# Kernel optimization log

Measured on AMD Instinct MI355X. Metric: run time of the kernel, lower is better.

Reference implementation:

```python
import jax, jax.numpy as jnp
import numpy as np

D_MODEL = 1024
N_HEADS = 16
N_KV_HEADS = 4
D_K = D_MODEL // N_HEADS
Q_SIZE = D_MODEL
KV_SIZE = N_KV_HEADS * D_K
QKV_SIZE = Q_SIZE + 2 * KV_SIZE
EPS = 1.1920929e-07  # torch.nn.RMSNorm default eps (fp32 machine eps)
ROPE_BASE = 10000.0


def rms_norm(x, w):
    # normalize over last dim, learned scale (torch nn.RMSNorm)
    return x * jax.lax.rsqrt(jnp.mean(x * x, axis=-1, keepdims=True) + EPS) * w


def rope(x):
    # torchtune RotaryPositionalEmbeddings: interleaved pairs, x is [B,T,H,D]
    T, d = x.shape[1], x.shape[-1]
    inv_freq = 1.0 / (ROPE_BASE ** (jnp.arange(0, d, 2, dtype=jnp.float32) / d))
    ang = jnp.arange(T, dtype=jnp.float32)[:, None] * inv_freq[None, :]  # [T, d/2]
    cos = jnp.cos(ang)[None, :, None, :]
    sin = jnp.sin(ang)[None, :, None, :]
    xr = x.reshape(x.shape[:-1] + (d // 2, 2))
    x1, x2 = xr[..., 0], xr[..., 1]
    out = jnp.stack([x1 * cos - x2 * sin, x1 * sin + x2 * cos], axis=-1)
    return out.reshape(x.shape)


def setup_inputs() -> dict:
    key = jax.random.key(0)
    k1, k2 = jax.random.split(key)
    x = jax.random.normal(k1, (2, 2048, D_MODEL), dtype=jnp.float32)
    qkvo = jax.random.normal(k2, (QKV_SIZE + D_MODEL, D_MODEL), dtype=jnp.float32) * 0.02
    q_norm_w = jnp.ones((D_K,), dtype=jnp.float32)
    k_norm_w = jnp.ones((D_K,), dtype=jnp.float32)
    return {"x": x, "qkvo": qkvo, "q_norm_w": q_norm_w, "k_norm_w": k_norm_w}


def reference(x, qkvo, q_norm_w, k_norm_w):
    B, T, _ = x.shape
    groups = N_HEADS // N_KV_HEADS
    qkv = x @ qkvo[:QKV_SIZE].T  # [B,T,qkv_size]
    Q = qkv[..., :Q_SIZE].reshape(B, T, N_HEADS, D_K)
    K = qkv[..., Q_SIZE:Q_SIZE + KV_SIZE].reshape(B, T, N_KV_HEADS, D_K)
    V = qkv[..., Q_SIZE + KV_SIZE:].reshape(B, T, N_KV_HEADS, D_K)
    Q = rope(rms_norm(Q, q_norm_w))
    K = rope(rms_norm(K, k_norm_w))
    K = jnp.repeat(K, groups, axis=2)  # GQA expand to [B,T,H,D]
    V = jnp.repeat(V, groups, axis=2)
    scale = 1.0 / np.sqrt(D_K).astype(np.float32)
    scores = jnp.einsum('bqhd,bkhd->bhqk', Q, K) * scale
    causal = jnp.tril(jnp.ones((T, T), dtype=bool))
    scores = jnp.where(causal[None, None], scores, jnp.float32(-jnp.inf))
    attn = jax.nn.softmax(scores, axis=-1)
    out = jnp.einsum('bhqk,bkhd->bqhd', attn, V).reshape(B, T, D_MODEL)
    return out @ qkvo[QKV_SIZE:].T
```

## Files before the change

### kernel.cpp

```cpp
#include <hip/hip_runtime.h>
#include <hip/hip_bf16.h>
#include <cstdint>
#include <cstddef>

typedef __bf16 bf16x8 __attribute__((ext_vector_type(8)));
typedef float f32x4 __attribute__((ext_vector_type(4)));

__device__ __forceinline__ unsigned short f2bf(float f) {
    unsigned u = __builtin_bit_cast(unsigned, f);
    u += 0x7FFFu + ((u >> 16) & 1u);
    return (unsigned short)(u >> 16);
}
__device__ __forceinline__ unsigned pk2(float a, float b) {
    typedef __bf16 bf16x2 __attribute__((ext_vector_type(2)));
    bf16x2 h;
    h[0] = (__bf16)a;
    h[1] = (__bf16)b;
    unsigned r;
    __builtin_memcpy(&r, &h, 4);
    return r;
}
__device__ __forceinline__ float fexp2(float x) {
#if __has_builtin(__builtin_amdgcn_exp2f)
    return __builtin_amdgcn_exp2f(x);
#else
    return __expf(x * 0.6931471805599453f);
#endif
}
__device__ __forceinline__ void gld16(const void* g, void* l) {
    __builtin_amdgcn_global_load_lds((const __attribute__((address_space(1))) void*)g,
                                     (__attribute__((address_space(3))) void*)l, 16, 0, 0);
}

__global__ __launch_bounds__(256) void cast_kernel(const float4* __restrict__ x,
                                                   const float4* __restrict__ w,
                                                   ushort4* __restrict__ xbf,
                                                   ushort4* __restrict__ wbf) {
    int i = blockIdx.x * 256 + threadIdx.x;
    const int NX4 = 4096 * 1024 / 4;
    const int NW4 = 2560 * 1024 / 4;
    float4 v;
    ushort4* o;
    if (i < NX4) { v = x[i]; o = xbf + i; }
    else {
        int j = i - NX4;
        if (j >= NW4) return;
        v = w[j]; o = wbf + j;
    }
    ushort4 r;
    r.x = f2bf(v.x); r.y = f2bf(v.y); r.z = f2bf(v.z); r.w = f2bf(v.w);
    *o = r;
}

__global__ __launch_bounds__(256) void gemm_bf16(const ushort* __restrict__ A,
                                                 const ushort* __restrict__ B,
                                                 float* __restrict__ C,
                                                 int M, int N, int K) {
    __shared__ __align__(16) ushort LA[2][4096];
    __shared__ __align__(16) ushort LB[2][8192];
    int tid = threadIdx.x;
    int w = tid >> 6, lane = tid & 63;
    int qm = lane & 15, quad = lane >> 4;
    int m0 = blockIdx.x * 64, n0 = blockIdx.y * 128;
    int mw = (w & 1) * 32, nw = (w >> 1) * 64;
    int sw = qm & 7;

    f32x4 acc[2][4];
#pragma unroll
    for (int i = 0; i < 2; i++)
#pragma unroll
        for (int j = 0; j < 4; j++) acc[i][j] = (f32x4){0.f, 0.f, 0.f, 0.f};

    int sa[2], ra[2], ga[2];
#pragma unroll
    for (int u = 0; u < 2; u++) {
        sa[u] = tid + u * 256;
        ra[u] = sa[u] >> 3;
        ga[u] = (sa[u] & 7) ^ (ra[u] & 7);
    }
    int sb[4], rb[4], gb[4];
#pragma unroll
    for (int u = 0; u < 4; u++) {
        sb[u] = tid + u * 256;
        rb[u] = sb[u] >> 3;
        gb[u] = (sb[u] & 7) ^ (rb[u] & 7);
    }

    auto do_stage = [&](int k0, int buf) {
#pragma unroll
        for (int u = 0; u < 2; u++)
            gld16(A + (size_t)(m0 + ra[u]) * K + k0 + ga[u] * 8, &LA[buf][sa[u] * 8]);
#pragma unroll
        for (int u = 0; u < 4; u++)
            gld16(B + (size_t)(n0 + rb[u]) * K + k0 + gb[u] * 8, &LB[buf][sb[u] * 8]);
    };

    do_stage(0, 0);
    int buf = 0;
    for (int k0 = 0; k0 < K; k0 += 64, buf ^= 1) {
        __syncthreads();
        if (k0 + 64 < K) do_stage(k0 + 64, buf ^ 1);
        bf16x8 a[2][2], bb[4][2];
#pragma unroll
        for (int mi = 0; mi < 2; mi++)
#pragma unroll
            for (int h = 0; h < 2; h++)
                a[mi][h] = *(const bf16x8*)&LA[buf][((mw + mi * 16 + qm) * 8 + ((h * 4 + quad) ^ sw)) * 8];
#pragma unroll
        for (int ni = 0; ni < 4; ni++)
#pragma unroll
            for (int h = 0; h < 2; h++)
                bb[ni][h] = *(const bf16x8*)&LB[buf][((nw + ni * 16 + qm) * 8 + ((h * 4 + quad) ^ sw)) * 8];
#pragma unroll
        for (int h = 0; h < 2; h++)
#pragma unroll
            for (int mi = 0; mi < 2; mi++)
#pragma unroll
                for (int ni = 0; ni < 4; ni++)
                    acc[mi][ni] = __builtin_amdgcn_mfma_f32_16x16x32_bf16(a[mi][h], bb[ni][h], acc[mi][ni], 0, 0, 0);
    }
#pragma unroll
    for (int mi = 0; mi < 2; mi++)
#pragma unroll
        for (int ni = 0; ni < 4; ni++) {
            int row = m0 + mw + mi * 16 + quad * 4;
            int col = n0 + nw + ni * 16 + qm;
            float* cp = C + (size_t)row * N + col;
#pragma unroll
            for (int r = 0; r < 4; r++) cp[(size_t)r * N] = acc[mi][ni][r];
        }
}

__global__ __launch_bounds__(256) void normrope_kernel(const float* __restrict__ qkv,
                                                       const float* __restrict__ qw,
                                                       const float* __restrict__ kw,
                                                       ushort* __restrict__ Q,
                                                       ushort* __restrict__ Kb) {
    int r = blockIdx.x;
    int b = r >> 11;
    int t = r & 2047;
    int tid = threadIdx.x;
    int w = tid >> 6;
    int lane = tid & 63;

    float inv_freq = __expf(-((float)(lane & 62) * (1.0f / 64.0f)) * 9.210340371976184f);
    float sn, cs;
    sincosf((float)t * inv_freq, &sn, &cs);

#pragma unroll
    for (int hg = 0; hg < 5; hg++) {
        int col = hg * 256 + w * 64 + lane;
        float v = qkv[(size_t)r * 1536 + col];
        float ss = v * v;
#pragma unroll
        for (int m = 1; m < 64; m <<= 1) ss += __shfl_xor(ss, m);
        float rinv = rsqrtf(ss * (1.0f / 64.0f) + 1.1920929e-7f);
        float wt = (hg < 4) ? qw[lane] : kw[lane];
        float vn = v * rinv * wt;
        float pr = __shfl_xor(vn, 1);
        float out = (lane & 1) ? fmaf(pr, sn, vn * cs) : fmaf(vn, cs, -pr * sn);
        if (hg < 4) {
            int h = hg * 4 + w;
            Q[((size_t)(b * 16 + h) * 2048 + t) * 64 + lane] = f2bf(out * 0.125f);
        } else {
            Kb[((size_t)(b * 4 + w) * 2048 + t) * 64 + lane] = f2bf(out);
        }
    }
}

__global__ __launch_bounds__(256) void vtrans_kernel(const float* __restrict__ qkv,
                                                     ushort* __restrict__ VT) {
    __shared__ float tile[64][65];
    int bkv = blockIdx.x;
    int t0 = blockIdx.y * 64;
    int b = bkv >> 2;
    int kvh = bkv & 3;
    int tid = threadIdx.x;
    int c = tid & 63;
    int rr = tid >> 6;
#pragma unroll
    for (int p = 0; p < 16; p++) {
        int tl = p * 4 + rr;
        tile[tl][c] = qkv[((size_t)(b * 2048) + t0 + tl) * 1536 + 1280 + kvh * 64 + c];
    }
    __syncthreads();
    int w5 = c & 31;
    int pc = (c & 32) + ((w5 >> 2) & 3) * 8 + (w5 >> 4) * 4 + (w5 & 3);
#pragma unroll
    for (int p = 0; p < 16; p++) {
        int dd = p * 4 + rr;
        VT[((size_t)bkv * 64 + dd) * 2048 + t0 + pc] = f2bf(tile[c][dd]);
    }
}

__global__ __launch_bounds__(256) void attn7_kernel(const ushort* __restrict__ Q,
                                                    const ushort* __restrict__ K,
                                                    const ushort* __restrict__ VT,
                                                    ushort* __restrict__ O) {
    __shared__ __align__(16) ushort KT[2][4096];
    __shared__ __align__(16) ushort VL[2][4096];

    const float LOG2E = 1.4426950408889634f;
    const float C8 = 11.541560327111707f;

    int blk = blockIdx.x;
    int qp = 31 - (blk >> 5);
    int bh = blk & 31;
    int tid = threadIdx.x;
    int w = tid >> 6, lane = tid & 63;
    int qm = lane & 15, quad = lane >> 4;
    int b = bh >> 4, h = bh & 15;
    int bkv = b * 4 + (h >> 2);

    const ushort* Qbh = Q + (size_t)bh * 2048 * 64;
    const ushort* Kbh = K + (size_t)bkv * 2048 * 64;
    const ushort* Vbh = VT + (size_t)bkv * 64 * 2048;
    int sw = qm & 7;

    int s0 = tid, s1 = tid + 256;
    int r0 = s0 >> 3, g0 = (s0 & 7) ^ (r0 & 7);
    int r1 = s1 >> 3, g1 = (s1 & 7) ^ (r1 & 7);

    auto do_stage = [&](int j0, int buf) {
        gld16(Kbh + (size_t)(j0 + r0) * 64 + g0 * 8, &KT[buf][s0 * 8]);
        gld16(Kbh + (size_t)(j0 + r1) * 64 + g1 * 8, &KT[buf][s1 * 8]);
        gld16(Vbh + (size_t)r0 * 2048 + j0 + g0 * 8, &VL[buf][s0 * 8]);
        gld16(Vbh + (size_t)r1 * 2048 + j0 + g1 * 8, &VL[buf][s1 * 8]);
    };

    int nch = qp + 1;
    int q0 = qp * 64 + w * 16;
    const ushort* qptr = Qbh + (size_t)(q0 + qm) * 64 + quad * 8;
    bf16x8 qb0 = *(const bf16x8*)qptr;
    bf16x8 qb1 = *(const bf16x8*)(qptr + 32);
    f32x4 oacc[4];
    float lacc = 0.f;
#pragma unroll
    for (int i = 0; i < 4; i++) oacc[i] = (f32x4){0.f, 0.f, 0.f, 0.f};

    do_stage(0, 0);
    int buf = 0;
#pragma unroll 1
    for (int i = 0; i < nch; i++, buf ^= 1) {
        int j0 = i * 64;
        __syncthreads();
        if (i + 1 < nch) do_stage(j0 + 64, buf ^ 1);

        f32x4 st[4];
#pragma unroll
        for (int tj = 0; tj < 4; tj++) st[tj] = (f32x4){0.f, 0.f, 0.f, 0.f};
#pragma unroll
        for (int tj = 0; tj < 4; tj++) {
            bf16x8 kf0 = *(const bf16x8*)&KT[buf][((16 * tj + qm) * 8 + (quad ^ sw)) * 8];
            bf16x8 kf1 = *(const bf16x8*)&KT[buf][((16 * tj + qm) * 8 + ((4 + quad) ^ sw)) * 8];
            st[tj] = __builtin_amdgcn_mfma_f32_16x16x32_bf16(kf0, qb0, st[tj], 0, 0, 0);
            st[tj] = __builtin_amdgcn_mfma_f32_16x16x32_bf16(kf1, qb1, st[tj], 0, 0, 0);
        }
        if (i == nch - 1) {
#pragma unroll
            for (int tj = 0; tj < 4; tj++)
#pragma unroll
                for (int r = 0; r < 4; r++) {
                    int key = j0 + tj * 16 + quad * 4 + r;
                    if (key > q0 + qm) st[tj][r] = -1e30f;
                }
        }
        float rs = 0.f;
#pragma unroll
        for (int tj = 0; tj < 4; tj++)
#pragma unroll
            for (int r = 0; r < 4; r++) {
                float pv = fexp2(fmaf(st[tj][r], LOG2E, -C8));
                st[tj][r] = pv;
                rs += pv;
            }
        lacc += rs;

        unsigned up[4];
        up[0] = pk2(st[0][0], st[0][1]);
        up[1] = pk2(st[0][2], st[0][3]);
        up[2] = pk2(st[1][0], st[1][1]);
        up[3] = pk2(st[1][2], st[1][3]);
        bf16x8 pf0;
        __builtin_memcpy(&pf0, up, 16);
        up[0] = pk2(st[2][0], st[2][1]);
        up[1] = pk2(st[2][2], st[2][3]);
        up[2] = pk2(st[3][0], st[3][1]);
        up[3] = pk2(st[3][2], st[3][3]);
        bf16x8 pf1;
        __builtin_memcpy(&pf1, up, 16);

#pragma unroll
        for (int dt = 0; dt < 4; dt++) {
            bf16x8 vf0 = *(const bf16x8*)&VL[buf][((16 * dt + qm) * 8 + (quad ^ sw)) * 8];
            bf16x8 vf1 = *(const bf16x8*)&VL[buf][((16 * dt + qm) * 8 + ((4 + quad) ^ sw)) * 8];
            oacc[dt] = __builtin_amdgcn_mfma_f32_16x16x32_bf16(vf0, pf0, oacc[dt], 0, 0, 0);
            oacc[dt] = __builtin_amdgcn_mfma_f32_16x16x32_bf16(vf1, pf1, oacc[dt], 0, 0, 0);
        }
    }
    float l = lacc;
    l += __shfl_xor(l, 16);
    l += __shfl_xor(l, 32);
    float rinv = 1.0f / l;
    uint2 val;
#pragma unroll
    for (int dt = 0; dt < 4; dt++) {
        val.x = pk2(oacc[dt][0] * rinv, oacc[dt][1] * rinv);
        val.y = pk2(oacc[dt][2] * rinv, oacc[dt][3] * rinv);
        *(uint2*)&O[((size_t)(b * 2048) + q0 + qm) * 1024 + h * 64 + dt * 16 + quad * 4] = val;
    }
}

extern "C" void kernel_launch(void* const* d_in, const int* in_sizes, int n_in,
                              void* d_out, int out_size, void* d_ws, size_t ws_size,
                              hipStream_t stream) {
    (void)in_sizes; (void)n_in; (void)out_size; (void)ws_size;
    const float* x    = (const float*)d_in[0];
    const float* qkvo = (const float*)d_in[1];
    const float* qw   = (const float*)d_in[2];
    const float* kw   = (const float*)d_in[3];
    float* out = (float*)d_out;

    char* ws = (char*)d_ws;
    ushort* xbf = (ushort*)(ws + 0);
    ushort* wbf = (ushort*)(ws + 8388608);
    float*  qkv = (float*)(ws + 13631488);
    ushort* Qb  = (ushort*)(ws + 38797312);
    ushort* Kb  = (ushort*)(ws + 47185920);
    ushort* VT  = (ushort*)(ws + 49283072);
    ushort* Ob  = (ushort*)(ws + 51380224);

    cast_kernel<<<6656, 256, 0, stream>>>((const float4*)x, (const float4*)qkvo,
                                          (ushort4*)xbf, (ushort4*)wbf);
    gemm_bf16<<<dim3(64, 12), 256, 0, stream>>>(xbf, wbf, qkv, 4096, 1536, 1024);
    normrope_kernel<<<4096, 256, 0, stream>>>(qkv, qw, kw, Qb, Kb);
    vtrans_kernel<<<dim3(8, 32), 256, 0, stream>>>(qkv, VT);
    attn7_kernel<<<1024, 256, 0, stream>>>(Qb, Kb, VT, Ob);
    gemm_bf16<<<dim3(64, 8), 256, 0, stream>>>(Ob, wbf + (size_t)1536 * 1024, out, 4096, 1024, 1024);
}
```

Measured before the change: 159.7 us.

## Enlarge GEMM tiles and process two query sub-tiles per warp in attention

The GEMM becomes a template with 128-row tiles and 96- or 128-column tiles, giving each warp a 4xRN MFMA block for more register reuse, with launch bounds asking for two blocks per CU. The attention kernel now gives each block 128 query rows, so each warp handles two 16-row sub-tiles that share the staged K and V tiles. Key chunks lying entirely past a warp's queries are skipped. This halves the grid sizes, which may reduce occupancy and load balance across CUs, and raises register pressure.

```diff
diff --git a/kernel.cpp b/kernel.cpp
--- a/kernel.cpp
+++ b/kernel.cpp
@@ -52,35 +52,36 @@
     *o = r;
 }
 
-__global__ __launch_bounds__(256) void gemm_bf16(const ushort* __restrict__ A,
-                                                 const ushort* __restrict__ B,
-                                                 float* __restrict__ C,
-                                                 int M, int N, int K) {
-    __shared__ __align__(16) ushort LA[2][4096];
-    __shared__ __align__(16) ushort LB[2][8192];
+template<int RN>
+__global__ __launch_bounds__(256, 2) void gemm_bf16(const ushort* __restrict__ A,
+                                                    const ushort* __restrict__ B,
+                                                    float* __restrict__ C,
+                                                    int M, int N, int K) {
+    __shared__ __align__(16) ushort LA[2][8192];
+    __shared__ __align__(16) ushort LB[2][RN * 2048];
     int tid = threadIdx.x;
     int w = tid >> 6, lane = tid & 63;
     int qm = lane & 15, quad = lane >> 4;
-    int m0 = blockIdx.x * 64, n0 = blockIdx.y * 128;
-    int mw = (w & 1) * 32, nw = (w >> 1) * 64;
+    int m0 = blockIdx.x * 128, n0 = blockIdx.y * (RN * 32);
+    int mw = (w & 1) * 64, nw = (w >> 1) * (RN * 16);
     int sw = qm & 7;
 
-    f32x4 acc[2][4];
-#pragma unroll
-    for (int i = 0; i < 2; i++)
-#pragma unroll
-        for (int j = 0; j < 4; j++) acc[i][j] = (f32x4){0.f, 0.f, 0.f, 0.f};
-
-    int sa[2], ra[2], ga[2];
-#pragma unroll
-    for (int u = 0; u < 2; u++) {
+    f32x4 acc[4][RN];
+#pragma unroll
+    for (int i = 0; i < 4; i++)
+#pragma unroll
+        for (int j = 0; j < RN; j++) acc[i][j] = (f32x4){0.f, 0.f, 0.f, 0.f};
+
+    int sa[4], ra[4], ga[4];
+#pragma unroll
+    for (int u = 0; u < 4; u++) {
         sa[u] = tid + u * 256;
         ra[u] = sa[u] >> 3;
         ga[u] = (sa[u] & 7) ^ (ra[u] & 7);
     }
-    int sb[4], rb[4], gb[4];
-#pragma unroll
-    for (int u = 0; u < 4; u++) {
+    int sb[RN], rb[RN], gb[RN];
+#pragma unroll
+    for (int u = 0; u < RN; u++) {
         sb[u] = tid + u * 256;
         rb[u] = sb[u] >> 3;
         gb[u] = (sb[u] & 7) ^ (rb[u] & 7);
@@ -88,10 +89,10 @@
 
     auto do_stage = [&](int k0, int buf) {
 #pragma unroll
-        for (int u = 0; u < 2; u++)
+        for (int u = 0; u < 4; u++)
             gld16(A + (size_t)(m0 + ra[u]) * K + k0 + ga[u] * 8, &LA[buf][sa[u] * 8]);
 #pragma unroll
-        for (int u = 0; u < 4; u++)
+        for (int u = 0; u < RN; u++)
             gld16(B + (size_t)(n0 + rb[u]) * K + k0 + gb[u] * 8, &LB[buf][sb[u] * 8]);
     };
 
@@ -100,29 +101,29 @@
     for (int k0 = 0; k0 < K; k0 += 64, buf ^= 1) {
         __syncthreads();
         if (k0 + 64 < K) do_stage(k0 + 64, buf ^ 1);
-        bf16x8 a[2][2], bb[4][2];
-#pragma unroll
-        for (int mi = 0; mi < 2; mi++)
+        bf16x8 a[4][2], bb[RN][2];
+#pragma unroll
+        for (int mi = 0; mi < 4; mi++)
 #pragma unroll
             for (int h = 0; h < 2; h++)
                 a[mi][h] = *(const bf16x8*)&LA[buf][((mw + mi * 16 + qm) * 8 + ((h * 4 + quad) ^ sw)) * 8];
 #pragma unroll
-        for (int ni = 0; ni < 4; ni++)
+        for (int ni = 0; ni < RN; ni++)
 #pragma unroll
             for (int h = 0; h < 2; h++)
                 bb[ni][h] = *(const bf16x8*)&LB[buf][((nw + ni * 16 + qm) * 8 + ((h * 4 + quad) ^ sw)) * 8];
 #pragma unroll
         for (int h = 0; h < 2; h++)
 #pragma unroll
-            for (int mi = 0; mi < 2; mi++)
-#pragma unroll
-                for (int ni = 0; ni < 4; ni++)
+            for (int mi = 0; mi < 4; mi++)
+#pragma unroll
+                for (int ni = 0; ni < RN; ni++)
                     acc[mi][ni] = __builtin_amdgcn_mfma_f32_16x16x32_bf16(a[mi][h], bb[ni][h], acc[mi][ni], 0, 0, 0);
     }
 #pragma unroll
-    for (int mi = 0; mi < 2; mi++)
-#pragma unroll
-        for (int ni = 0; ni < 4; ni++) {
+    for (int mi = 0; mi < 4; mi++)
+#pragma unroll
+        for (int ni = 0; ni < RN; ni++) {
             int row = m0 + mw + mi * 16 + quad * 4;
             int col = n0 + nw + ni * 16 + qm;
             float* cp = C + (size_t)row * N + col;
@@ -204,7 +205,7 @@
     const float C8 = 11.541560327111707f;
 
     int blk = blockIdx.x;
-    int qp = 31 - (blk >> 5);
+    int qp = 15 - (blk >> 5);
     int bh = blk & 31;
     int tid = threadIdx.x;
     int w = tid >> 6, lane = tid & 63;
@@ -228,15 +229,20 @@
         gld16(Vbh + (size_t)r1 * 2048 + j0 + g1 * 8, &VL[buf][s1 * 8]);
     };
 
-    int nch = qp + 1;
-    int q0 = qp * 64 + w * 16;
+    int nch = 2 * qp + 2;
+    int q0 = qp * 128 + w * 32;
     const ushort* qptr = Qbh + (size_t)(q0 + qm) * 64 + quad * 8;
-    bf16x8 qb0 = *(const bf16x8*)qptr;
-    bf16x8 qb1 = *(const bf16x8*)(qptr + 32);
-    f32x4 oacc[4];
-    float lacc = 0.f;
-#pragma unroll
-    for (int i = 0; i < 4; i++) oacc[i] = (f32x4){0.f, 0.f, 0.f, 0.f};
+    bf16x8 qb[2][2];
+    qb[0][0] = *(const bf16x8*)qptr;
+    qb[0][1] = *(const bf16x8*)(qptr + 32);
+    qb[1][0] = *(const bf16x8*)(qptr + 1024);
+    qb[1][1] = *(const bf16x8*)(qptr + 1056);
+    f32x4 oacc[2][4];
+    float lacc[2] = {0.f, 0.f};
+#pragma unroll
+    for (int t = 0; t < 2; t++)
+#pragma unroll
+        for (int i = 0; i < 4; i++) oacc[t][i] = (f32x4){0.f, 0.f, 0.f, 0.f};
 
     do_stage(0, 0);
     int buf = 0;
@@ -246,68 +252,84 @@
         __syncthreads();
         if (i + 1 < nch) do_stage(j0 + 64, buf ^ 1);
 
-        f32x4 st[4];
-#pragma unroll
-        for (int tj = 0; tj < 4; tj++) st[tj] = (f32x4){0.f, 0.f, 0.f, 0.f};
-#pragma unroll
-        for (int tj = 0; tj < 4; tj++) {
-            bf16x8 kf0 = *(const bf16x8*)&KT[buf][((16 * tj + qm) * 8 + (quad ^ sw)) * 8];
-            bf16x8 kf1 = *(const bf16x8*)&KT[buf][((16 * tj + qm) * 8 + ((4 + quad) ^ sw)) * 8];
-            st[tj] = __builtin_amdgcn_mfma_f32_16x16x32_bf16(kf0, qb0, st[tj], 0, 0, 0);
-            st[tj] = __builtin_amdgcn_mfma_f32_16x16x32_bf16(kf1, qb1, st[tj], 0, 0, 0);
+        if (j0 <= q0 + 31) {
+            f32x4 st[2][4];
+#pragma unroll
+            for (int t = 0; t < 2; t++)
+#pragma unroll
+                for (int tj = 0; tj < 4; tj++) st[t][tj] = (f32x4){0.f, 0.f, 0.f, 0.f};
+#pragma unroll
+            for (int tj = 0; tj < 4; tj++) {
+                bf16x8 kf0 = *(const bf16x8*)&KT[buf][((16 * tj + qm) * 8 + (quad ^ sw)) * 8];
+                bf16x8 kf1 = *(const bf16x8*)&KT[buf][((16 * tj + qm) * 8 + ((4 + quad) ^ sw)) * 8];
+#pragma unroll
+                for (int t = 0; t < 2; t++) {
+                    st[t][tj] = __builtin_amdgcn_mfma_f32_16x16x32_bf16(kf0, qb[t][0], st[t][tj], 0, 0, 0);
+                    st[t][tj] = __builtin_amdgcn_mfma_f32_16x16x32_bf16(kf1, qb[t][1], st[t][tj], 0, 0, 0);
+                }
+            }
+            if (j0 + 63 > q0) {
+#pragma unroll
+                for (int t = 0; t < 2; t++)
+#pragma unroll
+                    for (int tj = 0; tj < 4; tj++)
+#pragma unroll
+                        for (int r = 0; r < 4; r++) {
+                            int key = j0 + tj * 16 + quad * 4 + r;
+                            if (key > q0 + t * 16 + qm) st[t][tj][r] = -1e30f;
+                        }
+            }
+            bf16x8 pf[2][2];
+#pragma unroll
+            for (int t = 0; t < 2; t++) {
+                float rs = 0.f;
+#pragma unroll
+                for (int tj = 0; tj < 4; tj++)
+#pragma unroll
+                    for (int r = 0; r < 4; r++) {
+                        float pv = fexp2(fmaf(st[t][tj][r], LOG2E, -C8));
+                        st[t][tj][r] = pv;
+                        rs += pv;
+                    }
+                lacc[t] += rs;
+                unsigned up[4];
+                up[0] = pk2(st[t][0][0], st[t][0][1]);
+                up[1] = pk2(st[t][0][2], st[t][0][3]);
+                up[2] = pk2(st[t][1][0], st[t][1][1]);
+                up[3] = pk2(st[t][1][2], st[t][1][3]);
+                __builtin_memcpy(&pf[t][0], up, 16);
+                up[0] = pk2(st[t][2][0], st[t][2][1]);
+                up[1] = pk2(st[t][2][2], st[t][2][3]);
+                up[2] = pk2(st[t][3][0], st[t][3][1]);
+                up[3] = pk2(st[t][3][2], st[t][3][3]);
+                __builtin_memcpy(&pf[t][1], up, 16);
+            }
+
+#pragma unroll
+            for (int dt = 0; dt < 4; dt++) {
+                bf16x8 vf0 = *(const bf16x8*)&VL[buf][((16 * dt + qm) * 8 + (quad ^ sw)) * 8];
+                bf16x8 vf1 = *(const bf16x8*)&VL[buf][((16 * dt + qm) * 8 + ((4 + quad) ^ sw)) * 8];
+#pragma unroll
+                for (int t = 0; t < 2; t++) {
+                    oacc[t][dt] = __builtin_amdgcn_mfma_f32_16x16x32_bf16(vf0, pf[t][0], oacc[t][dt], 0, 0, 0);
+                    oacc[t][dt] = __builtin_amdgcn_mfma_f32_16x16x32_bf16(vf1, pf[t][1], oacc[t][dt], 0, 0, 0);
+                }
+            }
         }
-        if (i == nch - 1) {
-#pragma unroll
-            for (int tj = 0; tj < 4; tj++)
-#pragma unroll
-                for (int r = 0; r < 4; r++) {
-                    int key = j0 + tj * 16 + quad * 4 + r;
-                    if (key > q0 + qm) st[tj][r] = -1e30f;
-                }
+    }
+#pragma unroll
+    for (int t = 0; t < 2; t++) {
+        float l = lacc[t];
+        l += __shfl_xor(l, 16);
+        l += __shfl_xor(l, 32);
+        float rinv = 1.0f / l;
+        uint2 val;
+#pragma unroll
+        for (int dt = 0; dt < 4; dt++) {
+            val.x = pk2(oacc[t][dt][0] * rinv, oacc[t][dt][1] * rinv);
+            val.y = pk2(oacc[t][dt][2] * rinv, oacc[t][dt][3] * rinv);
+            *(uint2*)&O[((size_t)(b * 2048) + q0 + t * 16 + qm) * 1024 + h * 64 + dt * 16 + quad * 4] = val;
         }
-        float rs = 0.f;
-#pragma unroll
-        for (int tj = 0; tj < 4; tj++)
-#pragma unroll
-            for (int r = 0; r < 4; r++) {
-                float pv = fexp2(fmaf(st[tj][r], LOG2E, -C8));
-                st[tj][r] = pv;
-                rs += pv;
-            }
-        lacc += rs;
-
-        unsigned up[4];
-        up[0] = pk2(st[0][0], st[0][1]);
-        up[1] = pk2(st[0][2], st[0][3]);
-        up[2] = pk2(st[1][0], st[1][1]);
-        up[3] = pk2(st[1][2], st[1][3]);
-        bf16x8 pf0;
-        __builtin_memcpy(&pf0, up, 16);
-        up[0] = pk2(st[2][0], st[2][1]);
-        up[1] = pk2(st[2][2], st[2][3]);
-        up[2] = pk2(st[3][0], st[3][1]);
-        up[3] = pk2(st[3][2], st[3][3]);
-        bf16x8 pf1;
-        __builtin_memcpy(&pf1, up, 16);
-
-#pragma unroll
-        for (int dt = 0; dt < 4; dt++) {
-            bf16x8 vf0 = *(const bf16x8*)&VL[buf][((16 * dt + qm) * 8 + (quad ^ sw)) * 8];
-            bf16x8 vf1 = *(const bf16x8*)&VL[buf][((16 * dt + qm) * 8 + ((4 + quad) ^ sw)) * 8];
-            oacc[dt] = __builtin_amdgcn_mfma_f32_16x16x32_bf16(vf0, pf0, oacc[dt], 0, 0, 0);
-            oacc[dt] = __builtin_amdgcn_mfma_f32_16x16x32_bf16(vf1, pf1, oacc[dt], 0, 0, 0);
-        }
-    }
-    float l = lacc;
-    l += __shfl_xor(l, 16);
-    l += __shfl_xor(l, 32);
-    float rinv = 1.0f / l;
-    uint2 val;
-#pragma unroll
-    for (int dt = 0; dt < 4; dt++) {
-        val.x = pk2(oacc[dt][0] * rinv, oacc[dt][1] * rinv);
-        val.y = pk2(oacc[dt][2] * rinv, oacc[dt][3] * rinv);
-        *(uint2*)&O[((size_t)(b * 2048) + q0 + qm) * 1024 + h * 64 + dt * 16 + quad * 4] = val;
     }
 }
 
@@ -332,9 +354,9 @@
 
     cast_kernel<<<6656, 256, 0, stream>>>((const float4*)x, (const float4*)qkvo,
                                           (ushort4*)xbf, (ushort4*)wbf);
-    gemm_bf16<<<dim3(64, 12), 256, 0, stream>>>(xbf, wbf, qkv, 4096, 1536, 1024);
+    gemm_bf16<3><<<dim3(32, 16), 256, 0, stream>>>(xbf, wbf, qkv, 4096, 1536, 1024);
     normrope_kernel<<<4096, 256, 0, stream>>>(qkv, qw, kw, Qb, Kb);
     vtrans_kernel<<<dim3(8, 32), 256, 0, stream>>>(qkv, VT);
-    attn7_kernel<<<1024, 256, 0, stream>>>(Qb, Kb, VT, Ob);
-    gemm_bf16<<<dim3(64, 8), 256, 0, stream>>>(Ob, wbf + (size_t)1536 * 1024, out, 4096, 1024, 1024);
-}
+    attn7_kernel<<<512, 256, 0, stream>>>(Qb, Kb, VT, Ob);
+    gemm_bf16<4><<<dim3(32, 8), 256, 0, stream>>>(Ob, wbf + (size_t)1536 * 1024, out, 4096, 1024, 1024);
+}
```

Result: slower. 174.8 us (+9.5%).
